# Kernel optimization log

Hardware: AMD Instinct MI355X
Metric: run time of the kernel (lower is better)

Reference implementation:

```python
import jax, jax.numpy as jnp
import numpy as np

# Model dims (all-MiniLM-L6-v2 + repo config)
B, S = 32, 512          # batch, seq_len
D, H, HD = 384, 12, 32  # d_model, heads, head_dim
L, FF = 6, 1536         # layers, ffn hidden
V, P = 30522, 512       # vocab, max positions


def layer_norm(x, g, b, eps=1e-12):
    m = jnp.mean(x, -1, keepdims=True)
    v = jnp.var(x, -1, keepdims=True)
    return (x - m) * jax.lax.rsqrt(v + eps) * g + b


def deltanet(x, mask, Wq, bq, Wk, bk, Wv, bv, Wb, df, ds, mx, Wo, bo):
    # Hierarchical delta-rule linear attention: two decaying fast-weight states
    # (fast/slow) updated with the delta rule, mixed by a per-head gate.
    b_, s_, _ = x.shape
    q = (x @ Wq + bq).reshape(b_, s_, H, HD)
    k = (x @ Wk + bk).reshape(b_, s_, H, HD)
    v = (x @ Wv + bv).reshape(b_, s_, H, HD)
    q = q / (jnp.linalg.norm(q, axis=-1, keepdims=True) + 1e-6)
    k = k / (jnp.linalg.norm(k, axis=-1, keepdims=True) + 1e-6)
    beta = jax.nn.sigmoid(x @ Wb) * mask[..., None]   # [B,S,H] write strength
    a_f = jax.nn.sigmoid(df)    # [H] fast decay (~0.3 at init)
    a_s = jax.nn.sigmoid(ds)    # [H] slow decay (~0.85 at init)
    g = jax.nn.sigmoid(mx)      # [H] fast/slow mixing gate

    def step(carry, inp):
        Sf, Ss = carry          # each [B,H,HD_k,HD_v]
        qt, kt, vt, bt = inp    # [B,H,HD],[B,H,HD],[B,H,HD],[B,H]
        def upd(St, a):
            pred = jnp.einsum('bhkv,bhk->bhv', St, kt)
            outer = kt[..., :, None] * (vt - pred)[..., None, :]
            return a[None, :, None, None] * St + bt[..., None, None] * outer
        Sf = upd(Sf, a_f)
        Ss = upd(Ss, a_s)
        of = jnp.einsum('bhkv,bhk->bhv', Sf, qt)
        osl = jnp.einsum('bhkv,bhk->bhv', Ss, qt)
        ot = g[None, :, None] * of + (1.0 - g)[None, :, None] * osl
        return (Sf, Ss), ot

    xs = (q.transpose(1, 0, 2, 3), k.transpose(1, 0, 2, 3),
          v.transpose(1, 0, 2, 3), beta.transpose(1, 0, 2))
    S0 = jnp.zeros((b_, H, HD, HD), x.dtype)
    _, o = jax.lax.scan(step, (S0, S0), xs)
    o = o.transpose(1, 0, 2, 3).reshape(b_, s_, D)
    return o @ Wo + bo


def setup_inputs() -> dict:
    key = jax.random.key(0)
    ks = iter(jax.random.split(key, 64))
    n = lambda shape: jax.random.normal(next(ks), shape, jnp.float32) * 0.02
    inp = {
        'input_ids': jax.random.randint(next(ks), (B, S), 0, V),
        'attention_mask': jnp.ones((B, S), jnp.int32),
        'word_emb': n((V, D)),
        'pos_emb': n((P, D)),
        'type_emb': n((2, D)),
        'emb_ln_g': jnp.ones((D,), jnp.float32),
        'emb_ln_b': jnp.zeros((D,), jnp.float32),
        'Wq': n((L, D, D)), 'bq': jnp.zeros((L, D), jnp.float32),
        'Wk': n((L, D, D)), 'bk': jnp.zeros((L, D), jnp.float32),
        'Wv': n((L, D, D)), 'bv': jnp.zeros((L, D), jnp.float32),
        'Wb': n((L, D, H)),
        'decay_fast': jnp.full((L, H), float(np.log(0.3 / 0.7)), jnp.float32),
        'decay_slow': jnp.full((L, H), float(np.log(0.85 / 0.15)), jnp.float32),
        'mix_logit': jnp.zeros((L, H), jnp.float32),
        'Wo': n((L, D, D)), 'bo': jnp.zeros((L, D), jnp.float32),
        'attn_ln_g': jnp.ones((L, D), jnp.float32),
        'attn_ln_b': jnp.zeros((L, D), jnp.float32),
        'W1': n((L, D, FF)), 'b1': jnp.zeros((L, FF), jnp.float32),
        'W2': n((L, FF, D)), 'b2': jnp.zeros((L, D), jnp.float32),
        'ffn_ln_g': jnp.ones((L, D), jnp.float32),
        'ffn_ln_b': jnp.zeros((L, D), jnp.float32),
    }
    return inp


def reference(input_ids, attention_mask, word_emb, pos_emb, type_emb,
              emb_ln_g, emb_ln_b, Wq, bq, Wk, bk, Wv, bv, Wb,
              decay_fast, decay_slow, mix_logit, Wo, bo,
              attn_ln_g, attn_ln_b, W1, b1, W2, b2, ffn_ln_g, ffn_ln_b):
    mask = attention_mask.astype(jnp.float32)
    s = input_ids.shape[1]
    # BERT-style embeddings (token type 0 everywhere)
    x = word_emb[input_ids] + pos_emb[:s][None] + type_emb[0][None, None]
    x = layer_norm(x, emb_ln_g, emb_ln_b)
    for i in range(L):
        r = x
        xa = deltanet(x, mask, Wq[i], bq[i], Wk[i], bk[i], Wv[i], bv[i],
                      Wb[i], decay_fast[i], decay_slow[i], mix_logit[i],
                      Wo[i], bo[i])
        x = layer_norm(r + xa, attn_ln_g[i], attn_ln_b[i])
        r = x
        h = jax.nn.gelu(x @ W1[i] + b1[i])
        h = h @ W2[i] + b2[i]
        x = layer_norm(r + h, ffn_ln_g[i], ffn_ln_b[i])
    m = mask[..., None]
    pooled = jnp.sum(x * m, 1) / jnp.clip(jnp.sum(m, 1), 1e-9)
    return pooled / jnp.linalg.norm(pooled, axis=1, keepdims=True)
```

## Files before the change

### kernel.cpp

```cpp
#include <hip/hip_runtime.h>
#include <math.h>

#define HH 12
#define DD 384
#define SS 512
#define BBATCH 32
#define FFD 1536
#define MM (BBATCH*SS)
#define LL 6
#define NQKV 1280

typedef unsigned short u16;
typedef __attribute__((ext_vector_type(8))) __bf16 bf16x8;
typedef __attribute__((ext_vector_type(4))) float f32x4;

__device__ __forceinline__ float b2f(u16 u){ union{unsigned int i; float f;} x; x.i = ((unsigned int)u)<<16; return x.f; }
__device__ __forceinline__ u16 f2b(float f){
    union{unsigned int i; float f;} x; x.f = f; unsigned int i = x.i;
    return (u16)((i + 0x7fffu + ((i>>16)&1u)) >> 16);
}

__device__ __forceinline__ void async16(const float* g, float* ldsbase){
    __builtin_amdgcn_global_load_lds(
        (const __attribute__((address_space(1))) unsigned int*)g,
        (__attribute__((address_space(3))) unsigned int*)ldsbase, 16, 0, 0);
}

__global__ __launch_bounds__(256)
void tpose_f2b(const float* __restrict__ in, u16* __restrict__ out, int R, int C,
               size_t inL, size_t outL)
{
    __shared__ float tile[32][33];
    in  += (size_t)blockIdx.z * inL;
    out += (size_t)blockIdx.z * outL;
    int c0 = blockIdx.x*32, r0 = blockIdx.y*32;
    int tx = threadIdx.x & 31, ty = threadIdx.x >> 5;
    #pragma unroll
    for (int i=0;i<32;i+=8) tile[ty+i][tx] = in[(size_t)(r0+ty+i)*C + c0+tx];
    __syncthreads();
    #pragma unroll
    for (int i=0;i<32;i+=8) out[(size_t)(c0+ty+i)*R + r0+tx] = f2b(tile[tx][ty+i]);
}

__global__ __launch_bounds__(384)
void wb_pack(const float* __restrict__ Wb, u16* __restrict__ WqkvT)
{
    int i = blockIdx.x, c = threadIdx.x;
    const float* w = Wb + (size_t)i*DD*HH;
    u16* o = WqkvT + (size_t)i*NQKV*DD;
    #pragma unroll
    for (int j=0;j<HH;j++) o[(size_t)(3*DD+j)*DD + c] = f2b(w[(size_t)c*HH + j]);
}

__global__ __launch_bounds__(256)
void emb_ln(const int* __restrict__ ids, const float* __restrict__ we,
            const float* __restrict__ pe, const float* __restrict__ te,
            const float* __restrict__ g, const float* __restrict__ bta,
            float* __restrict__ xw, u16* __restrict__ xb)
{
    int row = blockIdx.x*4 + (threadIdx.x>>6); int s = row & 511;
    int l = threadIdx.x & 63;
    int id = ids[row];
    float x[6]; float sum=0.f, sq=0.f;
    #pragma unroll
    for (int i=0;i<6;i++){
        int c = l + 64*i;
        float v = we[(size_t)id*DD + c] + pe[(size_t)s*DD + c] + te[c];
        x[i]=v; sum+=v; sq+=v*v;
    }
    #pragma unroll
    for (int off=32; off; off>>=1){ sum += __shfl_xor(sum, off); sq += __shfl_xor(sq, off); }
    float m = sum*(1.0f/384.0f);
    float var = sq*(1.0f/384.0f) - m*m;
    float rs = rsqrtf(var + 1e-12f);
    #pragma unroll
    for (int i=0;i<6;i++){
        int c = l + 64*i;
        float y = (x[i]-m)*rs*g[c] + bta[c];
        xw[(size_t)row*DD + c] = y;
        xb[(size_t)row*DD + c] = f2b(y);
    }
}

__global__ __launch_bounds__(256)
void ln_res(float* __restrict__ xw, const u16* __restrict__ y,
            const float* __restrict__ g, const float* __restrict__ bta,
            u16* __restrict__ xb)
{
    int row = blockIdx.x*4 + (threadIdx.x>>6);
    int l = threadIdx.x & 63;
    float x[6]; float sum=0.f, sq=0.f;
    #pragma unroll
    for (int i=0;i<6;i++){
        int c = l + 64*i;
        float v = xw[(size_t)row*DD + c] + b2f(y[(size_t)row*DD + c]);
        x[i]=v; sum+=v; sq+=v*v;
    }
    #pragma unroll
    for (int off=32; off; off>>=1){ sum += __shfl_xor(sum, off); sq += __shfl_xor(sq, off); }
    float m = sum*(1.0f/384.0f);
    float var = sq*(1.0f/384.0f) - m*m;
    float rs = rsqrtf(var + 1e-12f);
    #pragma unroll
    for (int i=0;i<6;i++){
        int c = l + 64*i;
        float out = (x[i]-m)*rs*g[c] + bta[c];
        xw[(size_t)row*DD + c] = out;
        xb[(size_t)row*DD + c] = f2b(out);
    }
}

template<int EPI, int TM>
__global__ __launch_bounds__(256)
void gemm_bf16(const u16* __restrict__ A, const u16* __restrict__ Bt,
               const float* __restrict__ bias0, const float* __restrict__ bias1,
               const float* __restrict__ bias2,
               float* __restrict__ outF, u16* __restrict__ outB,
               const int* __restrict__ am, float* __restrict__ bet,
               int M, int N, int K)
{
    constexpr int MT = TM/32;
    __shared__ __align__(16) u16 As[2][TM*32];
    __shared__ __align__(16) u16 Bs[2][128*32];
    const int tid = threadIdx.x;
    const int m0 = blockIdx.y*TM, n0 = blockIdx.x*128;
    const int l  = tid & 63, w = tid >> 6;
    const int wm = (w>>1)*(TM/2), wn = (w&1)*64;
    const int lr = l & 15, lq = l >> 4;
    const int srow = l >> 2;
    const int scol = (l & 3) * 8;

    const int nk = K >> 5;
    auto prefetch = [&](int kk){
        int buf = kk & 1, k0 = kk << 5;
        if (TM == 128) {
            #pragma unroll
            for (int c = 0; c < 2; ++c) {
                int row = 32*w + 16*c + srow;
                async16((const float*)(A + (size_t)(m0+row)*K + k0 + scol),
                        (float*)&As[buf][(32*w + 16*c)*32]);
            }
        } else {
            int row = 16*w + srow;
            async16((const float*)(A + (size_t)(m0+row)*K + k0 + scol),
                    (float*)&As[buf][(16*w)*32]);
        }
        #pragma unroll
        for (int c = 0; c < 2; ++c) {
            int row = 32*w + 16*c + srow;
            async16((const float*)(Bt + (size_t)(n0+row)*K + k0 + scol),
                    (float*)&Bs[buf][(32*w + 16*c)*32]);
        }
    };

    f32x4 acc[MT][4] = {};
    prefetch(0);

    for (int kk = 0; kk < nk; ++kk) {
        int buf = kk & 1;
        __builtin_amdgcn_s_waitcnt(0);
        __syncthreads();
        if (kk+1 < nk) prefetch(kk+1);
        bf16x8 fa[MT], fb[4];
        #pragma unroll
        for (int mt=0; mt<MT; ++mt) fa[mt] = *(const bf16x8*)&As[buf][(wm+mt*16+lr)*32 + lq*8];
        #pragma unroll
        for (int nt=0; nt<4; ++nt) fb[nt] = *(const bf16x8*)&Bs[buf][(wn+nt*16+lr)*32 + lq*8];
        #pragma unroll
        for (int mt=0; mt<MT; ++mt)
            #pragma unroll
            for (int nt=0; nt<4; ++nt)
                acc[mt][nt] = __builtin_amdgcn_mfma_f32_16x16x32_bf16(fa[mt], fb[nt], acc[mt][nt], 0,0,0);
    }

    if constexpr (EPI == 2) {
        const int wq = n0 / DD;
        if (wq < 2) {
            const float* bias = (wq==0) ? bias0 : bias1;
            #pragma unroll
            for (int pr=0; pr<2; ++pr) {
                int nt0 = 2*pr, nt1 = nt0+1;
                int cc0 = (n0 - wq*DD) + wn + nt0*16 + lr;
                float bv0 = bias[cc0], bv1 = bias[cc0+16];
                int h = cc0 >> 5;
                #pragma unroll
                for (int mt=0; mt<MT; ++mt) {
                    int rb = m0 + wm + mt*16 + lq*4;
                    #pragma unroll
                    for (int r=0; r<4; ++r) {
                        float v0 = acc[mt][nt0][r] + bv0;
                        float v1 = acc[mt][nt1][r] + bv1;
                        float s2 = v0*v0 + v1*v1;
                        s2 += __shfl_xor(s2, 1); s2 += __shfl_xor(s2, 2);
                        s2 += __shfl_xor(s2, 4); s2 += __shfl_xor(s2, 8);
                        float sc = 1.0f/(sqrtf(s2) + 1e-6f);
                        int row = rb + r; int b = row >> 9, ss = row & 511;
                        size_t base = (size_t)wq*MM*DD + (((size_t)(b*HH+h))*SS + ss)*32;
                        outF[base + lr]      = v0*sc;
                        outF[base + lr + 16] = v1*sc;
                    }
                }
            }
        } else if (wq == 2) {
            #pragma unroll
            for (int nt=0; nt<4; ++nt) {
                int cc = (n0 - 2*DD) + wn + nt*16 + lr;
                float bv = bias2[cc];
                int h = cc >> 5, d = cc & 31;
                #pragma unroll
                for (int mt=0; mt<MT; ++mt) {
                    int rb = m0 + wm + mt*16 + lq*4;
                    #pragma unroll
                    for (int r=0; r<4; ++r) {
                        int row = rb + r; int b = row >> 9, ss = row & 511;
                        outF[(size_t)2*MM*DD + (((size_t)(b*HH+h))*SS + ss)*32 + d]
                            = acc[mt][nt][r] + bv;
                    }
                }
            }
        } else {
            #pragma unroll
            for (int nt=0; nt<4; ++nt) {
                int cc = wn + nt*16 + lr;
                if (cc < HH) {
                    #pragma unroll
                    for (int mt=0; mt<MT; ++mt) {
                        int rb = m0 + wm + mt*16 + lq*4;
                        #pragma unroll
                        for (int r=0; r<4; ++r) {
                            int row = rb + r; int b = row >> 9, ss = row & 511;
                            float vv = acc[mt][nt][r];
                            bet[((size_t)(b*HH+cc))*SS + ss] =
                                (1.0f/(1.0f+expf(-vv))) * (float)am[row];
                        }
                    }
                }
            }
        }
    } else {
        #pragma unroll
        for (int nt=0; nt<4; ++nt) {
            int col = n0 + wn + nt*16 + lr;
            float bv = bias0[col];
            #pragma unroll
            for (int mt=0; mt<MT; ++mt) {
                int rb = m0 + wm + mt*16 + lq*4;
                #pragma unroll
                for (int r=0; r<4; ++r) {
                    float v = acc[mt][nt][r] + bv;
                    int row = rb + r;
                    if (EPI == 0) {
                        outB[(size_t)row*N + col] = f2b(v);
                    } else {
                        float t = tanhf(0.7978845608028654f*(v + 0.044715f*v*v*v));
                        outB[(size_t)row*N + col] = f2b(0.5f*v*(1.0f+t));
                    }
                }
            }
        }
    }
}

#define EC 64
#define WU 48
#define NCH (SS/EC)
#define CH 16
__global__ __launch_bounds__(64, 3)
void scan(const float* __restrict__ qn, const float* __restrict__ kn,
          const float* __restrict__ vn, const float* __restrict__ beta,
          const float* __restrict__ df, const float* __restrict__ dsl,
          const float* __restrict__ mx, u16* __restrict__ o)
{
    __shared__ __align__(16) float ks[2][CH*32];
    __shared__ __align__(16) float qs[2][CH*32];
    __shared__ __align__(16) float vs[2][CH*32];
    __shared__ float bsh[2][CH];

    int blk = blockIdx.x;
    int nc = blk & (NCH-1); int bh = blk >> 3;
    int b = bh / HH, h = bh % HH;
    int l = threadIdx.x; int v = l & 31;
    float a_f = 1.0f/(1.0f+expf(-df[h]));
    float a_s = 1.0f/(1.0f+expf(-dsl[h]));
    float g   = 1.0f/(1.0f+expf(-mx[h]));
    float a = (l<32) ? a_f : a_s;
    const float* qb = qn + (size_t)bh*SS*32;
    const float* kb = kn + (size_t)bh*SS*32;
    const float* vb = vn + (size_t)bh*SS*32;
    const float* bb = beta + (size_t)bh*SS;
    u16* ob = o + ((size_t)b*SS*HH + h)*32 + v;

    const int tEmit  = nc*EC;
    const int tstart = (nc==0) ? 0 : tEmit - WU;
    const int nw     = (tEmit - tstart + EC)/CH;

    auto prefetch = [&](int w){
        int buf = w & 1;
        int t = tstart + w*CH;
        const float* kp = kb + (size_t)t*32;
        const float* vp = vb + (size_t)t*32;
        async16(kp + l*4,        &ks[buf][0]);
        async16(kp + 256 + l*4,  &ks[buf][256]);
        async16(vp + l*4,        &vs[buf][0]);
        async16(vp + 256 + l*4,  &vs[buf][256]);
        if (t >= tEmit){
            const float* qp = qb + (size_t)t*32;
            async16(qp + l*4,       &qs[buf][0]);
            async16(qp + 256 + l*4, &qs[buf][256]);
        }
        if (l < CH) bsh[buf][l] = bb[t + l];
    };

    prefetch(0);

    float S[32];
    #pragma unroll
    for (int j=0;j<32;j++) S[j]=0.f;

    for (int w=0; w<nw; ++w){
        __builtin_amdgcn_s_waitcnt(0);
        __syncthreads();
        if (w+1 < nw) prefetch(w+1);
        int buf = w & 1;
        int t = tstart + w*CH;
        if (t >= tEmit){
            for (int tt=0; tt<CH; ++tt){
                float kk[32];
                #pragma unroll
                for (int i=0;i<8;i++) *(float4*)&kk[i*4] = *(const float4*)&ks[buf][tt*32 + i*4];
                float vt = vs[buf][tt*32 + v];
                float bt = bsh[buf][tt];
                float p0=0.f,p1=0.f,p2=0.f,p3=0.f;
                #pragma unroll
                for (int j=0;j<32;j+=4){
                    p0+=S[j]*kk[j]; p1+=S[j+1]*kk[j+1]; p2+=S[j+2]*kk[j+2]; p3+=S[j+3]*kk[j+3];
                }
                float cc = bt*(vt - ((p0+p1)+(p2+p3)));
                float o0=0.f,o1=0.f,o2=0.f,o3=0.f;
                #pragma unroll
                for (int i=0;i<8;i++){
                    float4 q4 = *(const float4*)&qs[buf][tt*32 + i*4];
                    int j = i*4;
                    S[j]   = a*S[j]   + cc*kk[j];   o0 += S[j]*q4.x;
                    S[j+1] = a*S[j+1] + cc*kk[j+1]; o1 += S[j+1]*q4.y;
                    S[j+2] = a*S[j+2] + cc*kk[j+2]; o2 += S[j+2]*q4.z;
                    S[j+3] = a*S[j+3] + cc*kk[j+3]; o3 += S[j+3]*q4.w;
                }
                float ov  = (o0+o1)+(o2+o3);
                float oth = __shfl_xor(ov, 32);
                if (l < 32)
                    ob[(size_t)(t+tt)*HH*32] = f2b(g*ov + (1.0f-g)*oth);
            }
        } else {
            for (int tt=0; tt<CH; ++tt){
                float kk[32];
                #pragma unroll
                for (int i=0;i<8;i++) *(float4*)&kk[i*4] = *(const float4*)&ks[buf][tt*32 + i*4];
                float vt = vs[buf][tt*32 + v];
                float bt = bsh[buf][tt];
                float p0=0.f,p1=0.f,p2=0.f,p3=0.f;
                #pragma unroll
                for (int j=0;j<32;j+=4){
                    p0+=S[j]*kk[j]; p1+=S[j+1]*kk[j+1]; p2+=S[j+2]*kk[j+2]; p3+=S[j+3]*kk[j+3];
                }
                float cc = bt*(vt - ((p0+p1)+(p2+p3)));
                #pragma unroll
                for (int j=0;j<32;j+=4){
                    S[j]   = a*S[j]   + cc*kk[j];
                    S[j+1] = a*S[j+1] + cc*kk[j+1];
                    S[j+2] = a*S[j+2] + cc*kk[j+2];
                    S[j+3] = a*S[j+3] + cc*kk[j+3];
                }
            }
        }
        __syncthreads();
    }
}

__global__ __launch_bounds__(512)
void pool(const float* __restrict__ xw, const int* __restrict__ am, float* __restrict__ out)
{
    __shared__ float part[8][DD];
    __shared__ float cw[8];
    __shared__ float r2[8];
    int b = blockIdx.x, tid = threadIdx.x;
    int w = tid >> 6, l = tid & 63;
    float acc[6] = {0.f,0.f,0.f,0.f,0.f,0.f}; float cnt = 0.f;
    for (int s = w; s < SS; s += 8){
        float m = (float)am[b*SS+s]; cnt += m;
        const float* xr = xw + ((size_t)b*SS + s)*DD;
        #pragma unroll
        for (int i=0;i<6;i++) acc[i] += xr[l + 64*i]*m;
    }
    #pragma unroll
    for (int i=0;i<6;i++) part[w][l + 64*i] = acc[i];
    if (l == 0) cw[w] = cnt;
    __syncthreads();
    float mean = 0.f;
    if (tid < DD){
        float s = 0.f, c2 = 0.f;
        #pragma unroll
        for (int j=0;j<8;j++){ s += part[j][tid]; c2 += cw[j]; }
        mean = s / fmaxf(c2, 1e-9f);
    }
    float sq = (tid < DD) ? mean*mean : 0.f;
    #pragma unroll
    for (int off=32; off; off>>=1) sq += __shfl_xor(sq, off);
    __syncthreads();
    if (l == 0) r2[w] = sq;
    __syncthreads();
    if (tid == 0){
        float t = 0.f;
        #pragma unroll
        for (int j=0;j<8;j++) t += r2[j];
        r2[0] = 1.0f/sqrtf(t);
    }
    __syncthreads();
    if (tid < DD) out[(size_t)b*DD + tid] = mean * r2[0];
}

extern "C" void kernel_launch(void* const* d_in, const int* in_sizes, int n_in,
                              void* d_out, int out_size, void* d_ws, size_t ws_size,
                              hipStream_t stream)
{
    (void)in_sizes; (void)n_in; (void)out_size; (void)ws_size;
    const int*   ids = (const int*)d_in[0];
    const int*   am  = (const int*)d_in[1];
    const float* we  = (const float*)d_in[2];
    const float* pe  = (const float*)d_in[3];
    const float* te  = (const float*)d_in[4];
    const float* eg  = (const float*)d_in[5];
    const float* ebb = (const float*)d_in[6];
    const float* Wq  = (const float*)d_in[7];
    const float* bq  = (const float*)d_in[8];
    const float* Wk  = (const float*)d_in[9];
    const float* bk  = (const float*)d_in[10];
    const float* Wv  = (const float*)d_in[11];
    const float* bv  = (const float*)d_in[12];
    const float* Wb  = (const float*)d_in[13];
    const float* df  = (const float*)d_in[14];
    const float* dsl = (const float*)d_in[15];
    const float* mx  = (const float*)d_in[16];
    const float* Wo  = (const float*)d_in[17];
    const float* bo  = (const float*)d_in[18];
    const float* ag  = (const float*)d_in[19];
    const float* ab  = (const float*)d_in[20];
    const float* W1  = (const float*)d_in[21];
    const float* b1  = (const float*)d_in[22];
    const float* W2  = (const float*)d_in[23];
    const float* b2  = (const float*)d_in[24];
    const float* fg  = (const float*)d_in[25];
    const float* fb  = (const float*)d_in[26];

    char* p = (char*)d_ws;
    auto alloc = [&](size_t bytes)->char* {
        char* r = p; p += (bytes + 255) & ~(size_t)255; return r;
    };
    float* xw    = (float*)alloc((size_t)MM*DD*4);
    u16*   xb    = (u16*)  alloc((size_t)MM*DD*2);
    float* qkv   = (float*)alloc((size_t)3*MM*DD*4);
    u16*   obuf  = (u16*)  alloc((size_t)MM*DD*2);
    u16*   yout  = (u16*)  alloc((size_t)MM*DD*2);
    u16*   h1    = (u16*)  alloc((size_t)MM*FFD*2);
    float* bet   = (float*)alloc((size_t)BBATCH*HH*SS*4);
    u16*   WqkvT = (u16*)  alloc((size_t)LL*NQKV*DD*2);
    u16*   WoT   = (u16*)  alloc((size_t)LL*DD*DD*2);
    u16*   W1T   = (u16*)  alloc((size_t)LL*FFD*DD*2);
    u16*   W2T   = (u16*)  alloc((size_t)LL*DD*FFD*2);

    hipMemsetAsync(WqkvT, 0, (size_t)LL*NQKV*DD*2, stream);
    tpose_f2b<<<dim3(DD/32,  DD/32,  LL), 256, 0, stream>>>(Wq, WqkvT,            DD,  DD,  (size_t)DD*DD,  (size_t)NQKV*DD);
    tpose_f2b<<<dim3(DD/32,  DD/32,  LL), 256, 0, stream>>>(Wk, WqkvT + DD*DD,    DD,  DD,  (size_t)DD*DD,  (size_t)NQKV*DD);
    tpose_f2b<<<dim3(DD/32,  DD/32,  LL), 256, 0, stream>>>(Wv, WqkvT + 2*DD*DD,  DD,  DD,  (size_t)DD*DD,  (size_t)NQKV*DD);
    wb_pack<<<LL, 384, 0, stream>>>(Wb, WqkvT);
    tpose_f2b<<<dim3(DD/32,  DD/32,  LL), 256, 0, stream>>>(Wo, WoT,              DD,  DD,  (size_t)DD*DD,  (size_t)DD*DD);
    tpose_f2b<<<dim3(FFD/32, DD/32,  LL), 256, 0, stream>>>(W1, W1T,              DD,  FFD, (size_t)DD*FFD, (size_t)FFD*DD);
    tpose_f2b<<<dim3(DD/32,  FFD/32, LL), 256, 0, stream>>>(W2, W2T,              FFD, DD,  (size_t)FFD*DD, (size_t)DD*FFD);

    emb_ln<<<MM/4, 256, 0, stream>>>(ids, we, pe, te, eg, ebb, xw, xb);

    float* qn = qkv;
    float* kn = qkv + (size_t)MM*DD;
    float* vn = qkv + (size_t)2*MM*DD;

    for (int i = 0; i < LL; ++i) {
        gemm_bf16<2,128><<<dim3(NQKV/128, MM/128), 256, 0, stream>>>(
            xb, WqkvT + (size_t)i*NQKV*DD, bq + i*DD, bk + i*DD, bv + i*DD,
            qkv, nullptr, am, bet, MM, NQKV, DD);
        scan<<<BBATCH*HH*NCH, 64, 0, stream>>>(qn, kn, vn, bet,
            df + i*HH, dsl + i*HH, mx + i*HH, obuf);
        gemm_bf16<0,64><<<dim3(DD/128,  MM/64), 256, 0, stream>>>(
            obuf, WoT + (size_t)i*DD*DD, bo + i*DD, nullptr, nullptr,
            nullptr, yout, nullptr, nullptr, MM, DD, DD);
        ln_res<<<MM/4, 256, 0, stream>>>(xw, yout, ag + i*DD, ab + i*DD, xb);
        gemm_bf16<1,128><<<dim3(FFD/128, MM/128), 256, 0, stream>>>(
            xb, W1T + (size_t)i*FFD*DD, b1 + i*FFD, nullptr, nullptr,
            nullptr, h1, nullptr, nullptr, MM, FFD, DD);
        gemm_bf16<0,64><<<dim3(DD/128,  MM/64), 256, 0, stream>>>(
            h1, W2T + (size_t)i*DD*FFD, b2 + i*DD, nullptr, nullptr,
            nullptr, yout, nullptr, nullptr, MM, DD, FFD);
        ln_res<<<MM/4, 256, 0, stream>>>(xw, yout, fg + i*DD, fb + i*DD, xb);
    }

    pool<<<BBATCH, 512, 0, stream>>>(xw, am, (float*)d_out);
}
```

Measured before the change: 1.876 ms.

## Fuse output and FFN-down GEMMs with residual add and LayerNorm

Adds a gemm_ln kernel where each block computes a full 64x384 output tile, so the residual add, bias and LayerNorm can run in the epilogue. This drops the separate ln_res kernels and the bf16 yout intermediate, saving launches and a round trip through global memory. The tradeoff is only 256 blocks of one wave each, with heavy LDS use (about 56KB) and 24 accumulators per thread, which lowers occupancy and parallelism for the K=1536 GEMM. It also keeps the GEMM result in fp32 before the residual add instead of rounding it to bf16.

```diff
diff --git a/kernel.cpp b/kernel.cpp
--- a/kernel.cpp
+++ b/kernel.cpp
@@ -79,34 +79,6 @@
         float y = (x[i]-m)*rs*g[c] + bta[c];
         xw[(size_t)row*DD + c] = y;
         xb[(size_t)row*DD + c] = f2b(y);
-    }
-}
-
-__global__ __launch_bounds__(256)
-void ln_res(float* __restrict__ xw, const u16* __restrict__ y,
-            const float* __restrict__ g, const float* __restrict__ bta,
-            u16* __restrict__ xb)
-{
-    int row = blockIdx.x*4 + (threadIdx.x>>6);
-    int l = threadIdx.x & 63;
-    float x[6]; float sum=0.f, sq=0.f;
-    #pragma unroll
-    for (int i=0;i<6;i++){
-        int c = l + 64*i;
-        float v = xw[(size_t)row*DD + c] + b2f(y[(size_t)row*DD + c]);
-        x[i]=v; sum+=v; sq+=v*v;
-    }
-    #pragma unroll
-    for (int off=32; off; off>>=1){ sum += __shfl_xor(sum, off); sq += __shfl_xor(sq, off); }
-    float m = sum*(1.0f/384.0f);
-    float var = sq*(1.0f/384.0f) - m*m;
-    float rs = rsqrtf(var + 1e-12f);
-    #pragma unroll
-    for (int i=0;i<6;i++){
-        int c = l + 64*i;
-        float out = (x[i]-m)*rs*g[c] + bta[c];
-        xw[(size_t)row*DD + c] = out;
-        xb[(size_t)row*DD + c] = f2b(out);
     }
 }
 
@@ -249,14 +221,80 @@
                 for (int r=0; r<4; ++r) {
                     float v = acc[mt][nt][r] + bv;
                     int row = rb + r;
-                    if (EPI == 0) {
-                        outB[(size_t)row*N + col] = f2b(v);
-                    } else {
-                        float t = tanhf(0.7978845608028654f*(v + 0.044715f*v*v*v));
-                        outB[(size_t)row*N + col] = f2b(0.5f*v*(1.0f+t));
-                    }
-                }
-            }
+                    float t = tanhf(0.7978845608028654f*(v + 0.044715f*v*v*v));
+                    outB[(size_t)row*N + col] = f2b(0.5f*v*(1.0f+t));
+                }
+            }
+        }
+    }
+}
+
+__global__ __launch_bounds__(256, 1)
+void gemm_ln(const u16* __restrict__ A, const u16* __restrict__ Bt,
+             const float* __restrict__ bias,
+             const float* __restrict__ g, const float* __restrict__ bta,
+             float* __restrict__ xw, u16* __restrict__ xb, int K)
+{
+    __shared__ __align__(16) u16 As[2][64*32];
+    __shared__ __align__(16) u16 Bs[2][384*32];
+    const int tid = threadIdx.x;
+    const int m0 = blockIdx.x*64;
+    const int l  = tid & 63, w = tid >> 6;
+    const int lr = l & 15, lq = l >> 4;
+    const int srow = l >> 2, scol = (l & 3) * 8;
+
+    const int nk = K >> 5;
+    auto prefetch = [&](int kk){
+        int buf = kk & 1, k0 = kk << 5;
+        async16((const float*)(A + (size_t)(m0+16*w+srow)*K + k0 + scol),
+                (float*)&As[buf][(16*w)*32]);
+        #pragma unroll
+        for (int c2 = 0; c2 < 6; ++c2) {
+            int row = 96*w + 16*c2 + srow;
+            async16((const float*)(Bt + (size_t)row*K + k0 + scol),
+                    (float*)&Bs[buf][(96*w + 16*c2)*32]);
+        }
+    };
+
+    f32x4 acc[24] = {};
+    prefetch(0);
+
+    for (int kk = 0; kk < nk; ++kk) {
+        int buf = kk & 1;
+        __builtin_amdgcn_s_waitcnt(0);
+        __syncthreads();
+        if (kk+1 < nk) prefetch(kk+1);
+        bf16x8 fa = *(const bf16x8*)&As[buf][(16*w+lr)*32 + lq*8];
+        #pragma unroll
+        for (int nt=0; nt<24; ++nt) {
+            bf16x8 fb = *(const bf16x8*)&Bs[buf][(nt*16+lr)*32 + lq*8];
+            acc[nt] = __builtin_amdgcn_mfma_f32_16x16x32_bf16(fa, fb, acc[nt], 0,0,0);
+        }
+    }
+
+    #pragma unroll
+    for (int r=0; r<4; ++r) {
+        int row = m0 + 16*w + lq*4 + r;
+        float v[24]; float sum=0.f, sq=0.f;
+        #pragma unroll
+        for (int nt=0; nt<24; ++nt) {
+            int col = lr + 16*nt;
+            float x = xw[(size_t)row*DD + col] + acc[nt][r] + bias[col];
+            v[nt]=x; sum+=x; sq+=x*x;
+        }
+        sum += __shfl_xor(sum,1); sum += __shfl_xor(sum,2);
+        sum += __shfl_xor(sum,4); sum += __shfl_xor(sum,8);
+        sq  += __shfl_xor(sq,1);  sq  += __shfl_xor(sq,2);
+        sq  += __shfl_xor(sq,4);  sq  += __shfl_xor(sq,8);
+        float m  = sum*(1.0f/384.0f);
+        float var = sq*(1.0f/384.0f) - m*m;
+        float rs = rsqrtf(var + 1e-12f);
+        #pragma unroll
+        for (int nt=0; nt<24; ++nt) {
+            int col = lr + 16*nt;
+            float o = (v[nt]-m)*rs*g[col] + bta[col];
+            xw[(size_t)row*DD + col] = o;
+            xb[(size_t)row*DD + col] = f2b(o);
         }
     }
 }
@@ -460,7 +498,6 @@
     u16*   xb    = (u16*)  alloc((size_t)MM*DD*2);
     float* qkv   = (float*)alloc((size_t)3*MM*DD*4);
     u16*   obuf  = (u16*)  alloc((size_t)MM*DD*2);
-    u16*   yout  = (u16*)  alloc((size_t)MM*DD*2);
     u16*   h1    = (u16*)  alloc((size_t)MM*FFD*2);
     float* bet   = (float*)alloc((size_t)BBATCH*HH*SS*4);
     u16*   WqkvT = (u16*)  alloc((size_t)LL*NQKV*DD*2);
@@ -489,17 +526,15 @@
             qkv, nullptr, am, bet, MM, NQKV, DD);
         scan<<<BBATCH*HH*NCH, 64, 0, stream>>>(qn, kn, vn, bet,
             df + i*HH, dsl + i*HH, mx + i*HH, obuf);
-        gemm_bf16<0,64><<<dim3(DD/128,  MM/64), 256, 0, stream>>>(
-            obuf, WoT + (size_t)i*DD*DD, bo + i*DD, nullptr, nullptr,
-            nullptr, yout, nullptr, nullptr, MM, DD, DD);
-        ln_res<<<MM/4, 256, 0, stream>>>(xw, yout, ag + i*DD, ab + i*DD, xb);
+        gemm_ln<<<MM/64, 256, 0, stream>>>(
+            obuf, WoT + (size_t)i*DD*DD, bo + i*DD, ag + i*DD, ab + i*DD,
+            xw, xb, DD);
         gemm_bf16<1,128><<<dim3(FFD/128, MM/128), 256, 0, stream>>>(
             xb, W1T + (size_t)i*FFD*DD, b1 + i*FFD, nullptr, nullptr,
             nullptr, h1, nullptr, nullptr, MM, FFD, DD);
-        gemm_bf16<0,64><<<dim3(DD/128,  MM/64), 256, 0, stream>>>(
-            h1, W2T + (size_t)i*DD*FFD, b2 + i*DD, nullptr, nullptr,
-            nullptr, yout, nullptr, nullptr, MM, DD, FFD);
-        ln_res<<<MM/4, 256, 0, stream>>>(xw, yout, fg + i*DD, fb + i*DD, xb);
+        gemm_ln<<<MM/64, 256, 0, stream>>>(
+            h1, W2T + (size_t)i*DD*FFD, b2 + i*DD, fg + i*DD, fb + i*DD,
+            xw, xb, FFD);
     }
 
     pool<<<BBATCH, 512, 0, stream>>>(xw, am, (float*)d_out);
```

New measurement: 2.090 ms. 1.11x slower.
